# Kernel optimization log

Measured on AMD Instinct MI355X. Metric: run time of the kernel, lower is better.

Reference implementation:

```python
import jax, jax.numpy as jnp
import numpy as np


def setup_inputs() -> dict:
    key = jax.random.key(0)
    kq, kk, kv = jax.random.split(key, 3)
    B, S, D = 4, 4096, 128
    q = jax.random.normal(kq, (B, S, D), dtype=jnp.float32)
    k = jax.random.normal(kk, (B, S, D), dtype=jnp.float32)
    v = jax.random.normal(kv, (B, S, D), dtype=jnp.float32)
    return {"q": q, "k": k, "v": v}


def reference(q, k, v):
    # naive scaled dot-product attention: softmax(q k^T / sqrt(d)) v
    scale = 1.0 / jnp.sqrt(jnp.asarray(q.shape[-1], q.dtype))
    scores = jnp.einsum("bsd,btd->bst", q, k) * scale  # [B,S,S]
    probs = jax.nn.softmax(scores, axis=-1)
    out = jnp.einsum("bst,btd->bsd", probs, v)  # [B,S,Dv]
    return out
```

## Files before the change

### kernel.cpp

```cpp
#include <hip/hip_runtime.h>
#include <cmath>
#include <cstdint>

typedef __attribute__((ext_vector_type(8))) __bf16 bf16x8;
typedef __attribute__((ext_vector_type(16))) float f32x16;
typedef unsigned int u32;
typedef unsigned short u16;

constexpr int Bn = 4, Sn = 4096, Dn = 128;
constexpr int OSTR = 132;
constexpr float SCL2E = 0.08838834764831845f * 1.4426950408889634f;

__device__ __forceinline__ u32 pk2(float a, float b) {
  u32 r;
  asm("v_cvt_pk_bf16_f32 %0, %1, %2" : "=v"(r) : "v"(a), "v"(b));
  return r;
}

__device__ __forceinline__ void pl32swap(u32& a, u32& b) {
  asm("v_permlane32_swap_b32 %0, %1" : "+v"(a), "+v"(b));
}

__launch_bounds__(256)
__global__ void prep_kv(const float* __restrict__ Kg, const float* __restrict__ Vg,
                        u16* __restrict__ Kf, u16* __restrict__ Vf) {
  __shared__ float Tl[64 * 132];
  const int kt = blockIdx.x, b = blockIdx.y;
  const int tid = threadIdx.x;
  const size_t tileBase = ((size_t)b * 64 + kt) * 1024;

  #pragma unroll
  for (int r = 0; r < 8; ++r) {
    const int idx = tid + r * 256;
    const int row = idx >> 5, col = (idx & 31) * 4;
    float4 v = *(const float4*)(Kg + ((size_t)b * Sn + kt * 64 + row) * Dn + col);
    *(float4*)(Tl + row * 132 + col) = v;
  }
  __syncthreads();
  #pragma unroll
  for (int r = 0; r < 4; ++r) {
    const int g = tid + r * 256;
    const int c = g & 31, h = (g >> 5) & 1, tile = (g >> 6) & 1, kc = g >> 7;
    const float* s = Tl + (tile * 32 + c) * 132 + kc * 16 + h * 8;
    float4 f0 = *(const float4*)(s);
    float4 f1 = *(const float4*)(s + 4);
    uint4 o;
    o.x = pk2(f0.x, f0.y); o.y = pk2(f0.z, f0.w);
    o.z = pk2(f1.x, f1.y); o.w = pk2(f1.z, f1.w);
    *(uint4*)(Kf + (tileBase + g) * 8) = o;
  }
  __syncthreads();

  #pragma unroll
  for (int r = 0; r < 8; ++r) {
    const int idx = tid + r * 256;
    const int row = idx >> 5, col = (idx & 31) * 4;
    float4 v = *(const float4*)(Vg + ((size_t)b * Sn + kt * 64 + row) * Dn + col);
    *(float4*)(Tl + row * 132 + col) = v;
  }
  __syncthreads();
  #pragma unroll
  for (int r = 0; r < 4; ++r) {
    const int g = tid + r * 256;
    const int c = g & 31, h = (g >> 5) & 1, nt = (g >> 6) & 3, kc2 = g >> 8;
    const int key0 = kc2 * 16 + h * 8, dcol = nt * 32 + c;
    float x[8];
    #pragma unroll
    for (int j = 0; j < 8; ++j) x[j] = Tl[(key0 + j) * 132 + dcol];
    uint4 o;
    o.x = pk2(x[0], x[1]); o.y = pk2(x[2], x[3]);
    o.z = pk2(x[4], x[5]); o.w = pk2(x[6], x[7]);
    *(uint4*)(Vf + (tileBase + g) * 8) = o;
  }
}

__launch_bounds__(256, 2)
__global__ void attn_mfma(const float* __restrict__ qg, const u16* __restrict__ Kf,
                          const u16* __restrict__ Vf, float* __restrict__ Og) {
  __shared__ __align__(16) unsigned char lds[68608];
  float* Oc = (float*)lds;
  float* ml = (float*)(lds + 67584);

  const int tid = threadIdx.x;
  const int kp = tid >> 6, lane = tid & 63;
  const int c = lane & 31, h = lane >> 5;
  const int b = blockIdx.x & 3;
  const int q0 = (blockIdx.x >> 2) * 32;

  const u16* Kb = Kf + ((size_t)b * 64) * 1024 * 8;
  const u16* Vb = Vf + ((size_t)b * 64) * 1024 * 8;

  bf16x8 qf[8];
  {
    const float* Qr = qg + ((size_t)b * Sn + q0 + c) * Dn;
    #pragma unroll
    for (int kc = 0; kc < 8; ++kc) {
      float4 f0 = *(const float4*)(Qr + kc * 16 + h * 8);
      float4 f1 = *(const float4*)(Qr + kc * 16 + h * 8 + 4);
      uint4 t;
      t.x = pk2(f0.x * SCL2E, f0.y * SCL2E);
      t.y = pk2(f0.z * SCL2E, f0.w * SCL2E);
      t.z = pk2(f1.x * SCL2E, f1.y * SCL2E);
      t.w = pk2(f1.z * SCL2E, f1.w * SCL2E);
      qf[kc] = __builtin_bit_cast(bf16x8, t);
    }
  }

  f32x16 accO[4];
  #pragma unroll
  for (int nt = 0; nt < 4; ++nt)
    #pragma unroll
    for (int r = 0; r < 16; ++r) accO[nt][r] = 0.f;
  float l_i = 0.f;

  #pragma unroll 1
  for (int t8 = 0; t8 < 16; ++t8) {
    const int kt = kp * 16 + t8;
    const u16* Kt = Kb + (size_t)kt * 8192;
    const u16* Vt = Vb + (size_t)kt * 8192;

    uint4 ka[8], kb[8];
    #pragma unroll
    for (int kc = 0; kc < 4; ++kc) {
      ka[2 * kc + 0] = *(const uint4*)(Kt + (size_t)((kc * 4 + 0 + h) * 32 + c) * 8);
      ka[2 * kc + 1] = *(const uint4*)(Kt + (size_t)((kc * 4 + 2 + h) * 32 + c) * 8);
    }
    #pragma unroll
    for (int kc = 4; kc < 8; ++kc) {
      kb[2 * (kc - 4) + 0] = *(const uint4*)(Kt + (size_t)((kc * 4 + 0 + h) * 32 + c) * 8);
      kb[2 * (kc - 4) + 1] = *(const uint4*)(Kt + (size_t)((kc * 4 + 2 + h) * 32 + c) * 8);
    }

    f32x16 sa0, sa1;
    #pragma unroll
    for (int r = 0; r < 16; ++r) { sa0[r] = 0.f; sa1[r] = 0.f; }

    #pragma unroll
    for (int kc = 0; kc < 4; ++kc) {
      sa0 = __builtin_amdgcn_mfma_f32_32x32x16_bf16(__builtin_bit_cast(bf16x8, ka[2 * kc + 0]), qf[kc], sa0, 0, 0, 0);
      sa1 = __builtin_amdgcn_mfma_f32_32x32x16_bf16(__builtin_bit_cast(bf16x8, ka[2 * kc + 1]), qf[kc], sa1, 0, 0, 0);
    }

    uint4 va[8];
    #pragma unroll
    for (int kc2 = 0; kc2 < 2; ++kc2)
      #pragma unroll
      for (int nt = 0; nt < 4; ++nt)
        va[kc2 * 4 + nt] = *(const uint4*)(Vt + (size_t)((kc2 * 8 + nt * 2 + h) * 32 + c) * 8);

    #pragma unroll
    for (int kc = 4; kc < 8; ++kc) {
      sa0 = __builtin_amdgcn_mfma_f32_32x32x16_bf16(__builtin_bit_cast(bf16x8, kb[2 * (kc - 4) + 0]), qf[kc], sa0, 0, 0, 0);
      sa1 = __builtin_amdgcn_mfma_f32_32x32x16_bf16(__builtin_bit_cast(bf16x8, kb[2 * (kc - 4) + 1]), qf[kc], sa1, 0, 0, 0);
    }

    uint4 vb[8];
    #pragma unroll
    for (int kc2 = 2; kc2 < 4; ++kc2)
      #pragma unroll
      for (int nt = 0; nt < 4; ++nt)
        vb[(kc2 - 2) * 4 + nt] = *(const uint4*)(Vt + (size_t)((kc2 * 8 + nt * 2 + h) * 32 + c) * 8);

    float rs0 = 0.f, rs1 = 0.f;
    #pragma unroll
    for (int r = 0; r < 16; ++r) { sa0[r] = exp2f(sa0[r]); rs0 += sa0[r]; }
    #pragma unroll
    for (int r = 0; r < 16; ++r) { sa1[r] = exp2f(sa1[r]); rs1 += sa1[r]; }
    l_i += rs0 + rs1;

    u32 pk2v[2][8];
    #pragma unroll
    for (int i = 0; i < 8; ++i) {
      pk2v[0][i] = pk2(sa0[2 * i], sa0[2 * i + 1]);
      pk2v[1][i] = pk2(sa1[2 * i], sa1[2 * i + 1]);
    }

    #pragma unroll
    for (int kc2 = 0; kc2 < 4; ++kc2) {
      const int t = kc2 >> 1;
      const int bb = (kc2 & 1) * 4;
      u32 x0 = pk2v[t][bb], x1 = pk2v[t][bb + 1], x2 = pk2v[t][bb + 2], x3 = pk2v[t][bb + 3];
      pl32swap(x0, x2);
      pl32swap(x1, x3);
      uint4 afi; afi.x = x0; afi.y = x1; afi.z = x2; afi.w = x3;
      bf16x8 af = __builtin_bit_cast(bf16x8, afi);
      const uint4* vsrc = (kc2 < 2) ? &va[kc2 * 4] : &vb[(kc2 - 2) * 4];
      #pragma unroll
      for (int nt = 0; nt < 4; ++nt) {
        accO[nt] = __builtin_amdgcn_mfma_f32_32x32x16_bf16(__builtin_bit_cast(bf16x8, vsrc[nt]), af, accO[nt], 0, 0, 0);
      }
    }
  }

  l_i += __shfl_xor(l_i, 32);

  __syncthreads();
  {
    float* od = Oc + (size_t)(kp * 32) * OSTR;
    #pragma unroll
    for (int nt = 0; nt < 4; ++nt)
      #pragma unroll
      for (int r = 0; r < 16; ++r) {
        const int dr = (r & 3) + 8 * (r >> 2) + 4 * h;
        od[c * OSTR + nt * 32 + dr] = accO[nt][r];
      }
    if (h == 0) ml[kp * 32 + c] = l_i;
  }
  __syncthreads();
  {
    const int row = tid >> 3;
    const int d0 = (tid & 7) * 16;
    float lsum = 0.f;
    #pragma unroll
    for (int k2 = 0; k2 < 4; ++k2) lsum += ml[k2 * 32 + row];
    const float inv = 1.f / lsum;
    float4 acc[4];
    #pragma unroll
    for (int j = 0; j < 4; ++j) acc[j] = float4{0.f, 0.f, 0.f, 0.f};
    #pragma unroll
    for (int k2 = 0; k2 < 4; ++k2) {
      const float* oc = Oc + (size_t)(k2 * 32 + row) * OSTR + d0;
      #pragma unroll
      for (int j = 0; j < 4; ++j) {
        float4 vv = *(const float4*)(oc + 4 * j);
        acc[j].x += vv.x; acc[j].y += vv.y;
        acc[j].z += vv.z; acc[j].w += vv.w;
      }
    }
    float* op = Og + ((size_t)b * Sn + q0 + row) * Dn + d0;
    #pragma unroll
    for (int j = 0; j < 4; ++j) {
      float4 o = {acc[j].x * inv, acc[j].y * inv, acc[j].z * inv, acc[j].w * inv};
      *(float4*)(op + 4 * j) = o;
    }
  }
}

extern "C" void kernel_launch(void* const* d_in, const int* in_sizes, int n_in,
                              void* d_out, int out_size, void* d_ws, size_t ws_size,
                              hipStream_t stream) {
  const float* q = (const float*)d_in[0];
  const float* k = (const float*)d_in[1];
  const float* v = (const float*)d_in[2];
  float* out = (float*)d_out;
  const size_t N = (size_t)Bn * Sn * Dn;
  u16* Kf = (u16*)d_ws;
  u16* Vf = Kf + N;

  prep_kv<<<dim3(Sn / 64, Bn), dim3(256), 0, stream>>>(k, v, Kf, Vf);
  attn_mfma<<<dim3((Sn / 32) * Bn), dim3(256), 0, stream>>>(q, Kf, Vf, out);
}
```

Baseline: 123.8 us.

## Share K/V tiles in LDS across 8 query waves with split-K combine kernel

Result: slower. 129.3 us (+4.5%).

```diff
diff --git a/kernel.cpp b/kernel.cpp
--- a/kernel.cpp
+++ b/kernel.cpp
@@ -21,74 +21,74 @@
   asm("v_permlane32_swap_b32 %0, %1" : "+v"(a), "+v"(b));
 }
 
+__device__ __forceinline__ void gload_lds16(const void* g, void* l) {
+  __builtin_amdgcn_global_load_lds(
+      (const __attribute__((address_space(1))) u32*)g,
+      (__attribute__((address_space(3))) u32*)l, 16, 0, 0);
+}
+
 __launch_bounds__(256)
 __global__ void prep_kv(const float* __restrict__ Kg, const float* __restrict__ Vg,
                         u16* __restrict__ Kf, u16* __restrict__ Vf) {
   __shared__ float Tl[64 * 132];
-  const int kt = blockIdx.x, b = blockIdx.y;
+  const int kt = blockIdx.x, kind = blockIdx.y, b = blockIdx.z;
   const int tid = threadIdx.x;
   const size_t tileBase = ((size_t)b * 64 + kt) * 1024;
+  const float* src = (kind == 0 ? Kg : Vg) + ((size_t)b * Sn + kt * 64) * Dn;
 
   #pragma unroll
   for (int r = 0; r < 8; ++r) {
     const int idx = tid + r * 256;
     const int row = idx >> 5, col = (idx & 31) * 4;
-    float4 v = *(const float4*)(Kg + ((size_t)b * Sn + kt * 64 + row) * Dn + col);
+    float4 v = *(const float4*)(src + (size_t)row * Dn + col);
     *(float4*)(Tl + row * 132 + col) = v;
   }
   __syncthreads();
-  #pragma unroll
-  for (int r = 0; r < 4; ++r) {
-    const int g = tid + r * 256;
-    const int c = g & 31, h = (g >> 5) & 1, tile = (g >> 6) & 1, kc = g >> 7;
-    const float* s = Tl + (tile * 32 + c) * 132 + kc * 16 + h * 8;
-    float4 f0 = *(const float4*)(s);
-    float4 f1 = *(const float4*)(s + 4);
-    uint4 o;
-    o.x = pk2(f0.x, f0.y); o.y = pk2(f0.z, f0.w);
-    o.z = pk2(f1.x, f1.y); o.w = pk2(f1.z, f1.w);
-    *(uint4*)(Kf + (tileBase + g) * 8) = o;
-  }
-  __syncthreads();
-
-  #pragma unroll
-  for (int r = 0; r < 8; ++r) {
-    const int idx = tid + r * 256;
-    const int row = idx >> 5, col = (idx & 31) * 4;
-    float4 v = *(const float4*)(Vg + ((size_t)b * Sn + kt * 64 + row) * Dn + col);
-    *(float4*)(Tl + row * 132 + col) = v;
-  }
-  __syncthreads();
-  #pragma unroll
-  for (int r = 0; r < 4; ++r) {
-    const int g = tid + r * 256;
-    const int c = g & 31, h = (g >> 5) & 1, nt = (g >> 6) & 3, kc2 = g >> 8;
-    const int key0 = kc2 * 16 + h * 8, dcol = nt * 32 + c;
-    float x[8];
-    #pragma unroll
-    for (int j = 0; j < 8; ++j) x[j] = Tl[(key0 + j) * 132 + dcol];
-    uint4 o;
-    o.x = pk2(x[0], x[1]); o.y = pk2(x[2], x[3]);
-    o.z = pk2(x[4], x[5]); o.w = pk2(x[6], x[7]);
-    *(uint4*)(Vf + (tileBase + g) * 8) = o;
-  }
-}
-
-__launch_bounds__(256, 2)
-__global__ void attn_mfma(const float* __restrict__ qg, const u16* __restrict__ Kf,
-                          const u16* __restrict__ Vf, float* __restrict__ Og) {
-  __shared__ __align__(16) unsigned char lds[68608];
-  float* Oc = (float*)lds;
-  float* ml = (float*)(lds + 67584);
+  if (kind == 0) {
+    #pragma unroll
+    for (int r = 0; r < 4; ++r) {
+      const int g = tid + r * 256;
+      const int c = g & 31, h = (g >> 5) & 1, tile = (g >> 6) & 1, kc = g >> 7;
+      const float* s = Tl + (tile * 32 + c) * 132 + kc * 16 + h * 8;
+      float4 f0 = *(const float4*)(s);
+      float4 f1 = *(const float4*)(s + 4);
+      uint4 o;
+      o.x = pk2(f0.x, f0.y); o.y = pk2(f0.z, f0.w);
+      o.z = pk2(f1.x, f1.y); o.w = pk2(f1.z, f1.w);
+      *(uint4*)(Kf + (tileBase + g) * 8) = o;
+    }
+  } else {
+    #pragma unroll
+    for (int r = 0; r < 4; ++r) {
+      const int g = tid + r * 256;
+      const int c = g & 31, h = (g >> 5) & 1, nt = (g >> 6) & 3, kc2 = g >> 8;
+      const int key0 = kc2 * 16 + h * 8, dcol = nt * 32 + c;
+      float x[8];
+      #pragma unroll
+      for (int j = 0; j < 8; ++j) x[j] = Tl[(key0 + j) * 132 + dcol];
+      uint4 o;
+      o.x = pk2(x[0], x[1]); o.y = pk2(x[2], x[3]);
+      o.z = pk2(x[4], x[5]); o.w = pk2(x[6], x[7]);
+      *(uint4*)(Vf + (tileBase + g) * 8) = o;
+    }
+  }
+}
+
+__launch_bounds__(512)
+__global__ void attn_tile(const float* __restrict__ qg, const u16* __restrict__ Kf,
+                          const u16* __restrict__ Vf, float* __restrict__ Of,
+                          float* __restrict__ lw) {
+  __shared__ __align__(16) u16 kv[2][16384];
 
   const int tid = threadIdx.x;
-  const int kp = tid >> 6, lane = tid & 63;
+  const int w = tid >> 6, lane = tid & 63;
   const int c = lane & 31, h = lane >> 5;
-  const int b = blockIdx.x & 3;
-  const int q0 = (blockIdx.x >> 2) * 32;
-
-  const u16* Kb = Kf + ((size_t)b * 64) * 1024 * 8;
-  const u16* Vb = Vf + ((size_t)b * 64) * 1024 * 8;
+  const int bks = blockIdx.x & 15, qg2 = blockIdx.x >> 4;
+  const int b = bks >> 2, ks = bks & 3;
+  const int q0 = qg2 * 256 + w * 32;
+
+  const u16* Kb = Kf + ((size_t)b * 64 + ks * 16) * 1024 * 8;
+  const u16* Vb = Vf + ((size_t)b * 64 + ks * 16) * 1024 * 8;
 
   bf16x8 qf[8];
   {
@@ -113,6 +113,163 @@
     for (int r = 0; r < 16; ++r) accO[nt][r] = 0.f;
   float l_i = 0.f;
 
+  {
+    const u16* kt_ = Kb;
+    const u16* vt_ = Vb;
+    u16* lb = &kv[0][0];
+    #pragma unroll
+    for (int i = 0; i < 2; ++i)
+      gload_lds16(kt_ + i * 4096 + tid * 8, lb + i * 4096 + tid * 8);
+    #pragma unroll
+    for (int i = 0; i < 2; ++i)
+      gload_lds16(vt_ + i * 4096 + tid * 8, lb + 8192 + i * 4096 + tid * 8);
+  }
+  asm volatile("s_waitcnt vmcnt(0)" ::: "memory");
+  __syncthreads();
+
+  int cur = 0;
+  #pragma unroll 1
+  for (int t = 0; t < 16; ++t) {
+    if (t + 1 < 16) {
+      const u16* kt_ = Kb + (size_t)(t + 1) * 8192;
+      const u16* vt_ = Vb + (size_t)(t + 1) * 8192;
+      u16* lb = &kv[cur ^ 1][0];
+      #pragma unroll
+      for (int i = 0; i < 2; ++i)
+        gload_lds16(kt_ + i * 4096 + tid * 8, lb + i * 4096 + tid * 8);
+      #pragma unroll
+      for (int i = 0; i < 2; ++i)
+        gload_lds16(vt_ + i * 4096 + tid * 8, lb + 8192 + i * 4096 + tid * 8);
+    }
+
+    const u16* Ks = &kv[cur][0];
+    const u16* Vs = &kv[cur][8192];
+
+    f32x16 sa0, sa1;
+    #pragma unroll
+    for (int r = 0; r < 16; ++r) { sa0[r] = 0.f; sa1[r] = 0.f; }
+    #pragma unroll
+    for (int kc = 0; kc < 8; ++kc) {
+      uint4 a0 = *(const uint4*)(Ks + (size_t)((kc * 4 + 0 + h) * 32 + c) * 8);
+      uint4 a1 = *(const uint4*)(Ks + (size_t)((kc * 4 + 2 + h) * 32 + c) * 8);
+      sa0 = __builtin_amdgcn_mfma_f32_32x32x16_bf16(__builtin_bit_cast(bf16x8, a0), qf[kc], sa0, 0, 0, 0);
+      sa1 = __builtin_amdgcn_mfma_f32_32x32x16_bf16(__builtin_bit_cast(bf16x8, a1), qf[kc], sa1, 0, 0, 0);
+    }
+
+    float rs0 = 0.f, rs1 = 0.f;
+    #pragma unroll
+    for (int r = 0; r < 16; ++r) { sa0[r] = exp2f(sa0[r]); rs0 += sa0[r]; }
+    #pragma unroll
+    for (int r = 0; r < 16; ++r) { sa1[r] = exp2f(sa1[r]); rs1 += sa1[r]; }
+    l_i += rs0 + rs1;
+
+    u32 pk2v[2][8];
+    #pragma unroll
+    for (int i = 0; i < 8; ++i) {
+      pk2v[0][i] = pk2(sa0[2 * i], sa0[2 * i + 1]);
+      pk2v[1][i] = pk2(sa1[2 * i], sa1[2 * i + 1]);
+    }
+
+    #pragma unroll
+    for (int kc2 = 0; kc2 < 4; ++kc2) {
+      const int tt = kc2 >> 1;
+      const int bb = (kc2 & 1) * 4;
+      u32 x0 = pk2v[tt][bb], x1 = pk2v[tt][bb + 1], x2 = pk2v[tt][bb + 2], x3 = pk2v[tt][bb + 3];
+      pl32swap(x0, x2);
+      pl32swap(x1, x3);
+      uint4 afi; afi.x = x0; afi.y = x1; afi.z = x2; afi.w = x3;
+      bf16x8 af = __builtin_bit_cast(bf16x8, afi);
+      #pragma unroll
+      for (int nt = 0; nt < 4; ++nt) {
+        uint4 av = *(const uint4*)(Vs + (size_t)((kc2 * 8 + nt * 2 + h) * 32 + c) * 8);
+        accO[nt] = __builtin_amdgcn_mfma_f32_32x32x16_bf16(__builtin_bit_cast(bf16x8, av), af, accO[nt], 0, 0, 0);
+      }
+    }
+
+    asm volatile("s_waitcnt vmcnt(0)" ::: "memory");
+    __syncthreads();
+    cur ^= 1;
+  }
+
+  l_i += __shfl_xor(l_i, 32);
+  const size_t rowbase = (size_t)ks * 16384 + (size_t)b * 4096 + q0;
+  if (h == 0) lw[rowbase + c] = l_i;
+  float* op = Of + (rowbase + c) * 128;
+  #pragma unroll
+  for (int nt = 0; nt < 4; ++nt)
+    #pragma unroll
+    for (int rq = 0; rq < 4; ++rq) {
+      float4 wv = {accO[nt][4 * rq + 0], accO[nt][4 * rq + 1],
+                   accO[nt][4 * rq + 2], accO[nt][4 * rq + 3]};
+      *(float4*)(op + nt * 32 + rq * 8 + 4 * h) = wv;
+    }
+}
+
+__launch_bounds__(256)
+__global__ void combine(const float* __restrict__ Of, const float* __restrict__ lw,
+                        float* __restrict__ Og) {
+  const int gid = blockIdx.x * 256 + threadIdx.x;
+  const int row = gid >> 4;
+  const int d0 = (gid & 15) * 8;
+  float ls = 0.f;
+  #pragma unroll
+  for (int k2 = 0; k2 < 4; ++k2) ls += lw[(size_t)k2 * 16384 + row];
+  const float inv = 1.f / ls;
+  float a[8] = {0.f, 0.f, 0.f, 0.f, 0.f, 0.f, 0.f, 0.f};
+  #pragma unroll
+  for (int k2 = 0; k2 < 4; ++k2) {
+    const float* p = Of + ((size_t)k2 * 16384 + row) * 128 + d0;
+    float4 v0 = *(const float4*)(p);
+    float4 v1 = *(const float4*)(p + 4);
+    a[0] += v0.x; a[1] += v0.y; a[2] += v0.z; a[3] += v0.w;
+    a[4] += v1.x; a[5] += v1.y; a[6] += v1.z; a[7] += v1.w;
+  }
+  float* op = Og + (size_t)row * 128 + d0;
+  float4 o0 = {a[0] * inv, a[1] * inv, a[2] * inv, a[3] * inv};
+  float4 o1 = {a[4] * inv, a[5] * inv, a[6] * inv, a[7] * inv};
+  *(float4*)(op) = o0;
+  *(float4*)(op + 4) = o1;
+}
+
+__launch_bounds__(256, 2)
+__global__ void attn_legacy(const float* __restrict__ qg, const u16* __restrict__ Kf,
+                            const u16* __restrict__ Vf, float* __restrict__ Og) {
+  __shared__ __align__(16) unsigned char lds[68608];
+  float* Oc = (float*)lds;
+  float* ml = (float*)(lds + 67584);
+
+  const int tid = threadIdx.x;
+  const int kp = tid >> 6, lane = tid & 63;
+  const int c = lane & 31, h = lane >> 5;
+  const int b = blockIdx.x & 3;
+  const int q0 = (blockIdx.x >> 2) * 32;
+
+  const u16* Kb = Kf + ((size_t)b * 64) * 1024 * 8;
+  const u16* Vb = Vf + ((size_t)b * 64) * 1024 * 8;
+
+  bf16x8 qf[8];
+  {
+    const float* Qr = qg + ((size_t)b * Sn + q0 + c) * Dn;
+    #pragma unroll
+    for (int kc = 0; kc < 8; ++kc) {
+      float4 f0 = *(const float4*)(Qr + kc * 16 + h * 8);
+      float4 f1 = *(const float4*)(Qr + kc * 16 + h * 8 + 4);
+      uint4 t;
+      t.x = pk2(f0.x * SCL2E, f0.y * SCL2E);
+      t.y = pk2(f0.z * SCL2E, f0.w * SCL2E);
+      t.z = pk2(f1.x * SCL2E, f1.y * SCL2E);
+      t.w = pk2(f1.z * SCL2E, f1.w * SCL2E);
+      qf[kc] = __builtin_bit_cast(bf16x8, t);
+    }
+  }
+
+  f32x16 accO[4];
+  #pragma unroll
+  for (int nt = 0; nt < 4; ++nt)
+    #pragma unroll
+    for (int r = 0; r < 16; ++r) accO[nt][r] = 0.f;
+  float l_i = 0.f;
+
   #pragma unroll 1
   for (int t8 = 0; t8 < 16; ++t8) {
     const int kt = kp * 16 + t8;
@@ -134,26 +291,22 @@
     f32x16 sa0, sa1;
     #pragma unroll
     for (int r = 0; r < 16; ++r) { sa0[r] = 0.f; sa1[r] = 0.f; }
-
     #pragma unroll
     for (int kc = 0; kc < 4; ++kc) {
       sa0 = __builtin_amdgcn_mfma_f32_32x32x16_bf16(__builtin_bit_cast(bf16x8, ka[2 * kc + 0]), qf[kc], sa0, 0, 0, 0);
       sa1 = __builtin_amdgcn_mfma_f32_32x32x16_bf16(__builtin_bit_cast(bf16x8, ka[2 * kc + 1]), qf[kc], sa1, 0, 0, 0);
     }
-
     uint4 va[8];
     #pragma unroll
     for (int kc2 = 0; kc2 < 2; ++kc2)
       #pragma unroll
       for (int nt = 0; nt < 4; ++nt)
         va[kc2 * 4 + nt] = *(const uint4*)(Vt + (size_t)((kc2 * 8 + nt * 2 + h) * 32 + c) * 8);
-
     #pragma unroll
     for (int kc = 4; kc < 8; ++kc) {
       sa0 = __builtin_amdgcn_mfma_f32_32x32x16_bf16(__builtin_bit_cast(bf16x8, kb[2 * (kc - 4) + 0]), qf[kc], sa0, 0, 0, 0);
       sa1 = __builtin_amdgcn_mfma_f32_32x32x16_bf16(__builtin_bit_cast(bf16x8, kb[2 * (kc - 4) + 1]), qf[kc], sa1, 0, 0, 0);
     }
-
     uint4 vb[8];
     #pragma unroll
     for (int kc2 = 2; kc2 < 4; ++kc2)
@@ -193,7 +346,6 @@
   }
 
   l_i += __shfl_xor(l_i, 32);
-
   __syncthreads();
   {
     float* od = Oc + (size_t)(kp * 32) * OSTR;
@@ -246,7 +398,17 @@
   const size_t N = (size_t)Bn * Sn * Dn;
   u16* Kf = (u16*)d_ws;
   u16* Vf = Kf + N;
-
-  prep_kv<<<dim3(Sn / 64, Bn), dim3(256), 0, stream>>>(k, v, Kf, Vf);
-  attn_mfma<<<dim3((Sn / 32) * Bn), dim3(256), 0, stream>>>(q, Kf, Vf, out);
-}
+  float* Of = (float*)(Vf + N);
+  float* lwp = Of + 4 * N;
+  const size_t need = 4 * N
+                    + 4 * N * sizeof(float)
+                    + 4 * (size_t)Bn * Sn * sizeof(float);
+
+  prep_kv<<<dim3(Sn / 64, 2, Bn), dim3(256), 0, stream>>>(k, v, Kf, Vf);
+  if (ws_size >= need) {
+    attn_tile<<<dim3(256), dim3(512), 0, stream>>>(q, Kf, Vf, Of, lwp);
+    combine<<<dim3(1024), dim3(256), 0, stream>>>(Of, lwp, out);
+  } else {
+    attn_legacy<<<dim3((Sn / 32) * Bn), dim3(256), 0, stream>>>(q, Kf, Vf, out);
+  }
+}
```
